# Optimization experiments

Hardware: AMD Instinct MI355X
Metric: run time of the kernel (lower is better)

Reference implementation:

```python
import jax, jax.numpy as jnp
import numpy as np


def _silu(x):
    return x * jax.nn.sigmoid(x)


def setup_inputs() -> dict:
    key = jax.random.key(0)
    ks = jax.random.split(key, 8)
    B, S, H, E, I, IS = 2, 1024, 2048, 64, 512, 1024
    s = 0.02  # weight init scale to keep activations in a sane range
    return {
        "hidden_states": jax.random.normal(ks[0], (B, S, H), jnp.float32),
        "gate_weight": jax.random.normal(ks[1], (E, H), jnp.float32) * s,   # router [E,H]
        "w_gate": jax.random.normal(ks[2], (E, H, I), jnp.float32) * s,
        "w_up": jax.random.normal(ks[3], (E, H, I), jnp.float32) * s,
        "w_down": jax.random.normal(ks[4], (E, I, H), jnp.float32) * s,
        "sw_gate": jax.random.normal(ks[5], (H, IS), jnp.float32) * s,
        "sw_up": jax.random.normal(ks[6], (H, IS), jnp.float32) * s,
        "sw_down": jax.random.normal(ks[7], (IS, H), jnp.float32) * s,
        "top_k": 6,
    }


def reference(hidden_states, gate_weight, w_gate, w_up, w_down,
              sw_gate, sw_up, sw_down, top_k):
    orig_shape = hidden_states.shape
    H = orig_shape[-1]
    x = hidden_states.reshape(-1, H)          # [T,H]
    T = x.shape[0]
    E = gate_weight.shape[0]

    # fp32 router (need_fp32_gate)
    logits = x.astype(jnp.float32) @ gate_weight.astype(jnp.float32).T   # [T,E]
    # sigmoid_routing_function: sigmoid -> normalize -> topk -> renormalize
    p = jax.nn.sigmoid(logits)
    p = p / jnp.sum(p, axis=-1, keepdims=True)
    topk_w, topk_idx = jax.lax.top_k(p, top_k)                           # [T,k]
    topk_w = topk_w / jnp.sum(topk_w, axis=-1, keepdims=True)            # renormalize

    # dense combine weights [T,E]: zero for unselected experts
    cw = jnp.zeros((T, E), x.dtype).at[jnp.arange(T)[:, None], topk_idx].set(
        topk_w.astype(x.dtype))

    # grouped SwiGLU expert FFN, combine weighted outputs; scan over experts
    # keeps peak memory at one [T,I] intermediate per step.
    def step(acc, ew):
        wg, wu, wd, c = ew                                               # c: [T]
        y = (_silu(x @ wg) * (x @ wu)) @ wd                              # [T,H]
        return acc + c[:, None] * y, None

    routed, _ = jax.lax.scan(step, jnp.zeros_like(x),
                             (w_gate, w_up, w_down, cw.T))

    # shared experts FFN over all tokens (returned separately, not reduced)
    shared_out = (_silu(x @ sw_gate) * (x @ sw_up)) @ sw_down            # [T,H]

    return shared_out, routed.reshape(orig_shape)
```

## Files before the change

### kernel.cpp

```cpp
#include <hip/hip_runtime.h>
#include <hip/hip_bf16.h>
#include <stdint.h>


#define H_DIM 2048
#define E_NUM 64
#define I_DIM 512
#define IS_DIM 1024
#define CAPR 288
#define TOPK_MAX 8
#define BK 64
#define LDP 68

typedef float f32x4 __attribute__((ext_vector_type(4)));
typedef __bf16 bf16x8 __attribute__((ext_vector_type(8)));

__device__ __forceinline__ uint16_t f2bf(float f) {
  union { float f; uint32_t u; } v;
  v.f = f;
  uint32_t r = (v.u + 0x7FFFu + ((v.u >> 16) & 1u)) >> 16;
  return (uint16_t)r;
}
__device__ __forceinline__ uint32_t pack2(float a, float b) {
  return (uint32_t)f2bf(a) | ((uint32_t)f2bf(b) << 16);
}
__device__ __forceinline__ float bf2f(uint16_t b) {
  union { uint32_t u; float f; } v;
  v.u = (uint32_t)b << 16;
  return v.f;
}

#define BAR()                                              \
  do {                                                     \
    asm volatile("s_waitcnt lgkmcnt(0)" ::: "memory");     \
    __builtin_amdgcn_s_barrier();                          \
    asm volatile("" ::: "memory");                         \
  } while (0)

__global__ __launch_bounds__(256) void router_kernel(
    const float* __restrict__ x, const float* __restrict__ gw,
    const int* __restrict__ topk_ptr, int* __restrict__ cnt,
    int* __restrict__ bucket, float* __restrict__ bw,
    uint16_t* __restrict__ xbK, const int T) {
  const int t = blockIdx.x;
  const int tid = threadIdx.x;
  __shared__ float xs[H_DIM];
  __shared__ float logits[E_NUM];
#pragma unroll
  for (int i = 0; i < 2; ++i) {
    int idx = tid + i * 256;
    *(float4*)(&xs[idx * 4]) = *(const float4*)(x + (size_t)t * H_DIM + idx * 4);
  }
  __syncthreads();
  {
    const float* p = &xs[tid * 8];
    uint4 o;
    o.x = pack2(p[0], p[1]);
    o.y = pack2(p[2], p[3]);
    o.z = pack2(p[4], p[5]);
    o.w = pack2(p[6], p[7]);
    *(uint4*)(xbK + (size_t)(tid >> 2) * T * 32 + (size_t)t * 32 +
              (tid & 3) * 8) = o;
  }
  const int lane = tid & 63, wid = tid >> 6;
  float xr[32];
#pragma unroll
  for (int it = 0; it < 32; ++it) xr[it] = xs[lane + 64 * it];
  for (int eo = 0; eo < 16; ++eo) {
    int e = wid + eo * 4;
    const float* g = gw + (size_t)e * H_DIM;
    float acc = 0.f;
#pragma unroll
    for (int it = 0; it < 32; ++it) acc += xr[it] * g[lane + 64 * it];
#pragma unroll
    for (int off = 32; off; off >>= 1) acc += __shfl_xor(acc, off);
    if (lane == 0) logits[e] = acc;
  }
  __syncthreads();
  if (wid == 0) {
    int k = topk_ptr[0];
    if (k > TOPK_MAX) k = TOPK_MAX;
    float v = 1.f / (1.f + expf(-logits[lane]));
    float s = 0.f, myw = 0.f;
    int mye = 0;
    for (int j = 0; j < k; ++j) {
      float m = v;
      int mi = lane;
#pragma unroll
      for (int off = 32; off; off >>= 1) {
        float ov = __shfl_xor(m, off);
        int oi = __shfl_xor(mi, off);
        if (ov > m || (ov == m && oi < mi)) { m = ov; mi = oi; }
      }
      if (lane == j) { myw = m; mye = mi; }
      if (lane == mi) v = -1e30f;
      s += m;
    }
    if (lane < k) {
      float w = myw / s;
      int pos = atomicAdd(&cnt[mye], 1);
      if (pos < CAPR) {
        bucket[mye * CAPR + pos] = t * 8 + lane;
        bw[mye * CAPR + pos] = w;
      }
    }
  }
}

__global__ __launch_bounds__(256) void gather_xe(
    const uint16_t* __restrict__ xbK, const int* __restrict__ cnt,
    const int* __restrict__ bucket, uint16_t* __restrict__ xe, const int T) {
  const int e = blockIdx.x;
  const int kgrp = blockIdx.y & 15, sgrp = blockIdx.y >> 4;
  const int tid = threadIdx.x;
  const int slot = sgrp * 64 + (tid & 63);
  const int kblk = kgrp * 4 + (tid >> 6);
  const int n_e = min(cnt[e], CAPR);
  if (slot >= n_e) return;
  const int t = bucket[e * CAPR + slot] >> 3;
  const uint4* src = (const uint4*)(xbK + (size_t)kblk * T * 32 + (size_t)t * 32);
  uint4* dst = (uint4*)(xe + (size_t)e * (64 * CAPR * 32) +
                        (size_t)kblk * (CAPR * 32) + (size_t)slot * 32);
#pragma unroll
  for (int j = 0; j < 4; ++j) dst[j] = src[j];
}

template <int BM, bool GATHER>
__global__ __launch_bounds__(256) void ffn_in(
    const uint16_t* __restrict__ A0, const float* __restrict__ Wg,
    const float* __restrict__ Wu, uint16_t* __restrict__ actO,
    const int* __restrict__ cnt, const int K, const int ldb, const int SLOTS) {
  constexpr int BN = 32;
  constexpr int MF = BM / 64;
  constexpr int NF = 2;

  int e = 0, nt, mt0, mtE, n_e;
  const float *Bg, *Bu;
  const uint16_t* AE;
  uint16_t* outE;
  if constexpr (GATHER) {
    e = blockIdx.x;
    nt = blockIdx.y;
    n_e = min(cnt[e], CAPR);
    mt0 = 0;
    mtE = (n_e + BM - 1) / BM;
    const size_t wo = (size_t)e * K * ldb;
    Bg = Wg + wo;
    Bu = Wu + wo;
    AE = A0 + (size_t)e * (64 * CAPR * 32);
    outE = actO + (size_t)e * ((I_DIM / 32) * CAPR * 32);
  } else {
    nt = blockIdx.x;
    mt0 = blockIdx.y;
    mtE = mt0 + 1;
    n_e = 1 << 30;
    Bg = Wg;
    Bu = Wu;
    AE = A0;
    outE = actO;
  }
  if (mt0 * BM >= n_e) return;

  __shared__ uint16_t Bgs[2][BN][LDP];
  __shared__ uint16_t Bus[2][BN][LDP];

  const int tid = threadIdx.x;
  const int cg4 = (tid & 7) * 4, kp = tid >> 3;
  const float* bgp = Bg + (size_t)(2 * kp) * ldb + nt * BN + cg4;
  const float* bup = Bu + (size_t)(2 * kp) * ldb + nt * BN + cg4;

  const int lane = tid & 63, wid = tid >> 6;
  const int fr = lane & 15, kg = lane >> 4;
  const int wrow = wid * (BM / 4);
  const size_t ldA = (size_t)SLOTS * 32;

  float4 g0, g1, u0, u1;
  const int NS = K / BK;

  for (int mt = mt0; mt < mtE; ++mt) {
    const uint16_t* ab[MF];
#pragma unroll
    for (int mf = 0; mf < MF; ++mf)
      ab[mf] = AE + (size_t)(mt * BM + wrow + mf * 16 + fr) * 32 + kg * 8;

    f32x4 accg[MF][NF] = {};
    f32x4 accu[MF][NF] = {};

    g0 = *(const float4*)bgp;
    g1 = *(const float4*)(bgp + ldb);
    u0 = *(const float4*)bup;
    u1 = *(const float4*)(bup + ldb);
    {
      const int k2 = 2 * kp;
      *(uint32_t*)(&Bgs[0][cg4 + 0][k2]) = pack2(g0.x, g1.x);
      *(uint32_t*)(&Bgs[0][cg4 + 1][k2]) = pack2(g0.y, g1.y);
      *(uint32_t*)(&Bgs[0][cg4 + 2][k2]) = pack2(g0.z, g1.z);
      *(uint32_t*)(&Bgs[0][cg4 + 3][k2]) = pack2(g0.w, g1.w);
      *(uint32_t*)(&Bus[0][cg4 + 0][k2]) = pack2(u0.x, u1.x);
      *(uint32_t*)(&Bus[0][cg4 + 1][k2]) = pack2(u0.y, u1.y);
      *(uint32_t*)(&Bus[0][cg4 + 2][k2]) = pack2(u0.z, u1.z);
      *(uint32_t*)(&Bus[0][cg4 + 3][k2]) = pack2(u0.w, u1.w);
    }
    if (NS > 1) {
      const float* g = bgp + (size_t)BK * ldb;
      g0 = *(const float4*)g;
      g1 = *(const float4*)(g + ldb);
      const float* u = bup + (size_t)BK * ldb;
      u0 = *(const float4*)u;
      u1 = *(const float4*)(u + ldb);
    }
    BAR();

    int b = 0;
    for (int s = 0; s < NS; ++s) {
      uint4 a[MF][2];
#pragma unroll
      for (int mf = 0; mf < MF; ++mf)
#pragma unroll
        for (int sl = 0; sl < 2; ++sl)
          a[mf][sl] = *(const uint4*)(ab[mf] + (size_t)(2 * s + sl) * ldA);
      if (s + 1 < NS) {
        const int k2 = 2 * kp;
        *(uint32_t*)(&Bgs[b ^ 1][cg4 + 0][k2]) = pack2(g0.x, g1.x);
        *(uint32_t*)(&Bgs[b ^ 1][cg4 + 1][k2]) = pack2(g0.y, g1.y);
        *(uint32_t*)(&Bgs[b ^ 1][cg4 + 2][k2]) = pack2(g0.z, g1.z);
        *(uint32_t*)(&Bgs[b ^ 1][cg4 + 3][k2]) = pack2(g0.w, g1.w);
        *(uint32_t*)(&Bus[b ^ 1][cg4 + 0][k2]) = pack2(u0.x, u1.x);
        *(uint32_t*)(&Bus[b ^ 1][cg4 + 1][k2]) = pack2(u0.y, u1.y);
        *(uint32_t*)(&Bus[b ^ 1][cg4 + 2][k2]) = pack2(u0.z, u1.z);
        *(uint32_t*)(&Bus[b ^ 1][cg4 + 3][k2]) = pack2(u0.w, u1.w);
      }
      if (s + 2 < NS) {
        const float* g = bgp + (size_t)((s + 2) * BK) * ldb;
        g0 = *(const float4*)g;
        g1 = *(const float4*)(g + ldb);
        const float* u = bup + (size_t)((s + 2) * BK) * ldb;
        u0 = *(const float4*)u;
        u1 = *(const float4*)(u + ldb);
      }
#pragma unroll
      for (int sl = 0; sl < 2; ++sl)
#pragma unroll
        for (int nf = 0; nf < NF; ++nf) {
          const bf16x8 bg = __builtin_bit_cast(
              bf16x8, *(const uint4*)(&Bgs[b][nf * 16 + fr][kg * 8 + sl * 32]));
          const bf16x8 bu = __builtin_bit_cast(
              bf16x8, *(const uint4*)(&Bus[b][nf * 16 + fr][kg * 8 + sl * 32]));
#pragma unroll
          for (int mf = 0; mf < MF; ++mf) {
            const bf16x8 af = __builtin_bit_cast(bf16x8, a[mf][sl]);
            accg[mf][nf] = __builtin_amdgcn_mfma_f32_16x16x32_bf16(
                af, bg, accg[mf][nf], 0, 0, 0);
            accu[mf][nf] = __builtin_amdgcn_mfma_f32_16x16x32_bf16(
                af, bu, accu[mf][nf], 0, 0, 0);
          }
        }
      BAR();
      b ^= 1;
    }

#pragma unroll
    for (int mf = 0; mf < MF; ++mf)
#pragma unroll
      for (int rr = 0; rr < 4; ++rr) {
        const int slot = mt * BM + wrow + mf * 16 + kg * 4 + rr;
        if (slot < n_e) {
          uint16_t* op = outE + (size_t)nt * ldA + (size_t)slot * 32 + fr;
#pragma unroll
          for (int nf = 0; nf < NF; ++nf) {
            const float g = accg[mf][nf][rr], u = accu[mf][nf][rr];
            op[nf * 16] = f2bf(g / (1.f + expf(-g)) * u);
          }
        }
      }
  }
}

template <int BM, bool GATHER>
__global__ __launch_bounds__(256) void ffn_down(
    const uint16_t* __restrict__ A0, const float* __restrict__ Wd,
    void* __restrict__ outp, const int* __restrict__ cnt,
    const int* __restrict__ bucket, const float* __restrict__ bw,
    const int K, const int SLOTS) {
  constexpr int BN = 64;
  constexpr int MF = BM / 64;
  constexpr int NF = 4;

  int e = 0, nt, mt0, mtE, n_e;
  const float* Bd;
  const uint16_t* AE;
  if constexpr (GATHER) {
    e = blockIdx.x;
    nt = blockIdx.y;
    n_e = min(cnt[e], CAPR);
    mt0 = 0;
    mtE = (n_e + BM - 1) / BM;
    AE = A0 + (size_t)e * ((I_DIM / 32) * CAPR * 32);
    Bd = Wd + (size_t)e * K * H_DIM;
  } else {
    nt = blockIdx.x;
    mt0 = blockIdx.y;
    mtE = mt0 + 1;
    n_e = 1 << 30;
    AE = A0;
    Bd = Wd;
  }
  if (mt0 * BM >= n_e) return;

  __shared__ uint16_t Bs[2][BN][LDP];

  const int tid = threadIdx.x;
  const int cg4 = (tid & 15) * 4, kp = tid >> 4;
  const float* bdp = Bd + (size_t)(2 * kp) * H_DIM + nt * BN + cg4;

  const int lane = tid & 63, wid = tid >> 6;
  const int fr = lane & 15, kg = lane >> 4;
  const int wrow = wid * (BM / 4);
  const size_t ldA = (size_t)SLOTS * 32;

  float4 d0[2], d1[2];
  const int NS = K / BK;

  for (int mt = mt0; mt < mtE; ++mt) {
    const uint16_t* ab[MF];
#pragma unroll
    for (int mf = 0; mf < MF; ++mf)
      ab[mf] = AE + (size_t)(mt * BM + wrow + mf * 16 + fr) * 32 + kg * 8;

    f32x4 acc[MF][NF] = {};

#pragma unroll
    for (int pp = 0; pp < 2; ++pp) {
      const float* d = bdp + (size_t)(2 * pp * 16) * H_DIM;
      d0[pp] = *(const float4*)d;
      d1[pp] = *(const float4*)(d + H_DIM);
    }
#pragma unroll
    for (int pp = 0; pp < 2; ++pp) {
      const int k2 = 2 * (kp + pp * 16);
      *(uint32_t*)(&Bs[0][cg4 + 0][k2]) = pack2(d0[pp].x, d1[pp].x);
      *(uint32_t*)(&Bs[0][cg4 + 1][k2]) = pack2(d0[pp].y, d1[pp].y);
      *(uint32_t*)(&Bs[0][cg4 + 2][k2]) = pack2(d0[pp].z, d1[pp].z);
      *(uint32_t*)(&Bs[0][cg4 + 3][k2]) = pack2(d0[pp].w, d1[pp].w);
    }
    if (NS > 1) {
#pragma unroll
      for (int pp = 0; pp < 2; ++pp) {
        const float* d = bdp + (size_t)(BK + 2 * pp * 16) * H_DIM;
        d0[pp] = *(const float4*)d;
        d1[pp] = *(const float4*)(d + H_DIM);
      }
    }
    BAR();

    int b = 0;
    for (int s = 0; s < NS; ++s) {
      uint4 a[MF][2];
#pragma unroll
      for (int mf = 0; mf < MF; ++mf)
#pragma unroll
        for (int sl = 0; sl < 2; ++sl)
          a[mf][sl] = *(const uint4*)(ab[mf] + (size_t)(2 * s + sl) * ldA);
      if (s + 1 < NS) {
#pragma unroll
        for (int pp = 0; pp < 2; ++pp) {
          const int k2 = 2 * (kp + pp * 16);
          *(uint32_t*)(&Bs[b ^ 1][cg4 + 0][k2]) = pack2(d0[pp].x, d1[pp].x);
          *(uint32_t*)(&Bs[b ^ 1][cg4 + 1][k2]) = pack2(d0[pp].y, d1[pp].y);
          *(uint32_t*)(&Bs[b ^ 1][cg4 + 2][k2]) = pack2(d0[pp].z, d1[pp].z);
          *(uint32_t*)(&Bs[b ^ 1][cg4 + 3][k2]) = pack2(d0[pp].w, d1[pp].w);
        }
      }
      if (s + 2 < NS) {
#pragma unroll
        for (int pp = 0; pp < 2; ++pp) {
          const float* d = bdp + (size_t)((s + 2) * BK + 2 * pp * 16) * H_DIM;
          d0[pp] = *(const float4*)d;
          d1[pp] = *(const float4*)(d + H_DIM);
        }
      }
#pragma unroll
      for (int sl = 0; sl < 2; ++sl)
#pragma unroll
        for (int nf = 0; nf < NF; ++nf) {
          const bf16x8 bf_ = __builtin_bit_cast(
              bf16x8, *(const uint4*)(&Bs[b][nf * 16 + fr][kg * 8 + sl * 32]));
#pragma unroll
          for (int mf = 0; mf < MF; ++mf) {
            const bf16x8 af = __builtin_bit_cast(bf16x8, a[mf][sl]);
            acc[mf][nf] = __builtin_amdgcn_mfma_f32_16x16x32_bf16(
                af, bf_, acc[mf][nf], 0, 0, 0);
          }
        }
      BAR();
      b ^= 1;
    }

    const int col0 = nt * BN + fr;
#pragma unroll
    for (int mf = 0; mf < MF; ++mf)
#pragma unroll
      for (int rr = 0; rr < 4; ++rr) {
        const int slot = mt * BM + wrow + mf * 16 + kg * 4 + rr;
        if constexpr (GATHER) {
          if (slot < n_e) {
            const int bv = bucket[e * CAPR + slot];
            const float w = bw[e * CAPR + slot];
            uint16_t* yb = (uint16_t*)outp + (size_t)bv * H_DIM + col0;
#pragma unroll
            for (int nf = 0; nf < NF; ++nf)
              yb[nf * 16] = f2bf(w * acc[mf][nf][rr]);
          }
        } else {
          float* op = (float*)outp + (size_t)slot * H_DIM + col0;
#pragma unroll
          for (int nf = 0; nf < NF; ++nf) op[nf * 16] = acc[mf][nf][rr];
        }
      }
  }
}

__global__ __launch_bounds__(256) void combine_kernel(
    const uint16_t* __restrict__ ybuf, const int* __restrict__ topk_ptr,
    float* __restrict__ routed) {
  const int t = blockIdx.x;
  const int tid = threadIdx.x;
  int k = topk_ptr[0];
  if (k > TOPK_MAX) k = TOPK_MAX;
  float acc[8] = {};
  const uint16_t* base = ybuf + (size_t)t * 8 * H_DIM + tid * 8;
  for (int j = 0; j < k; ++j) {
    uint4 v = *(const uint4*)(base + (size_t)j * H_DIM);
    const uint16_t* h = (const uint16_t*)&v;
#pragma unroll
    for (int i = 0; i < 8; ++i) acc[i] += bf2f(h[i]);
  }
  float* op = routed + (size_t)t * H_DIM + tid * 8;
  *(float4*)op = make_float4(acc[0], acc[1], acc[2], acc[3]);
  *(float4*)(op + 4) = make_float4(acc[4], acc[5], acc[6], acc[7]);
}

extern "C" void kernel_launch(void* const* d_in, const int* in_sizes, int n_in,
                              void* d_out, int out_size, void* d_ws, size_t ws_size,
                              hipStream_t stream) {
  const float* x = (const float*)d_in[0];
  const float* gw = (const float*)d_in[1];
  const float* w_gate = (const float*)d_in[2];
  const float* w_up = (const float*)d_in[3];
  const float* w_down = (const float*)d_in[4];
  const float* sw_gate = (const float*)d_in[5];
  const float* sw_up = (const float*)d_in[6];
  const float* sw_down = (const float*)d_in[7];
  const int* topk = (const int*)d_in[8];
  const int T = in_sizes[0] / H_DIM;

  float* shared_out = (float*)d_out;
  float* routed = shared_out + (size_t)T * H_DIM;

  char* ws = (char*)d_ws;
  size_t off = 0;
  auto take = [&](size_t b) {
    char* p = ws + off;
    off += (b + 255) & ~(size_t)255;
    return p;
  };
  uint16_t* xbK = (uint16_t*)take((size_t)T * H_DIM * 2);
  int* cnt = (int*)take(E_NUM * 4);
  int* bucket = (int*)take((size_t)E_NUM * CAPR * 4);
  float* bw = (float*)take((size_t)E_NUM * CAPR * 4);
  uint16_t* xe = (uint16_t*)take((size_t)E_NUM * 64 * CAPR * 32 * 2 + 65536);
  uint16_t* act = (uint16_t*)take((size_t)E_NUM * 16 * CAPR * 32 * 2 + 65536);
  uint16_t* s_act = (uint16_t*)take((size_t)(IS_DIM / 32) * T * 32 * 2);
  uint16_t* ybuf = (uint16_t*)take((size_t)T * 8 * H_DIM * 2);

  hipMemsetAsync(cnt, 0, E_NUM * 4, stream);

  router_kernel<<<T, 256, 0, stream>>>(x, gw, topk, cnt, bucket, bw, xbK, T);
  gather_xe<<<dim3(E_NUM, 16 * ((CAPR + 63) / 64)), 256, 0, stream>>>(
      xbK, cnt, bucket, xe, T);

  ffn_in<256, true><<<dim3(E_NUM, I_DIM / 32), 256, 0, stream>>>(
      xe, w_gate, w_up, act, cnt, H_DIM, I_DIM, CAPR);
  ffn_down<256, true><<<dim3(E_NUM, H_DIM / 64), 256, 0, stream>>>(
      act, w_down, (void*)ybuf, cnt, bucket, bw, I_DIM, CAPR);
  combine_kernel<<<T, 256, 0, stream>>>(ybuf, topk, routed);
  ffn_in<128, false><<<dim3(IS_DIM / 32, T / 128), 256, 0, stream>>>(
      xbK, sw_gate, sw_up, s_act, nullptr, H_DIM, IS_DIM, T);
  ffn_down<128, false><<<dim3(H_DIM / 64, T / 128), 256, 0, stream>>>(
      s_act, sw_down, (void*)shared_out, nullptr, nullptr, nullptr, IS_DIM, T);
}
```

Measured before the change: 440.5 us.

## Unroll GEMM k-loop by two with prefetched A registers and hardware bf16 pack

Both expert GEMM kernels (gate/up and down) now unroll the k-loop by two. They keep two register sets for the B tiles and two for the A fragments, so the A loads for the next step are issued before the barrier instead of at the top of each iteration. The software round-to-nearest bf16 conversion is replaced with the v_cvt_pk_bf16_f32 instruction. The aim is to hide global A-load latency behind the MFMAs and cut VALU work in the B packing. The cost is higher register pressure, which may lower occupancy. The loop assumes NS is even, or relies on guards when it is not.

```diff
diff --git a/kernel.cpp b/kernel.cpp
--- a/kernel.cpp
+++ b/kernel.cpp
@@ -23,6 +23,11 @@
 }
 __device__ __forceinline__ uint32_t pack2(float a, float b) {
   return (uint32_t)f2bf(a) | ((uint32_t)f2bf(b) << 16);
+}
+__device__ __forceinline__ uint32_t cvtpk(float a, float b) {
+  uint32_t r;
+  asm("v_cvt_pk_bf16_f32 %0, %1, %2" : "=v"(r) : "v"(a), "v"(b));
+  return r;
 }
 __device__ __forceinline__ float bf2f(uint16_t b) {
   union { uint32_t u; float f; } v;
@@ -174,89 +179,92 @@
   const int wrow = wid * (BM / 4);
   const size_t ldA = (size_t)SLOTS * 32;
 
-  float4 g0, g1, u0, u1;
+  struct BSet { float4 g0, g1, u0, u1; };
+  BSet bs0, bs1;
+  uint4 aA[MF][2], aB[MF][2];
+  const uint16_t* ab[MF];
+
+  auto issueB = [&](BSet& S, int kq) {
+    const float* g = bgp + (size_t)kq * ldb;
+    S.g0 = *(const float4*)g;
+    S.g1 = *(const float4*)(g + ldb);
+    const float* u = bup + (size_t)kq * ldb;
+    S.u0 = *(const float4*)u;
+    S.u1 = *(const float4*)(u + ldb);
+  };
+  auto packB = [&](int buf, const BSet& S) {
+    const int k2 = 2 * kp;
+    *(uint32_t*)(&Bgs[buf][cg4 + 0][k2]) = cvtpk(S.g0.x, S.g1.x);
+    *(uint32_t*)(&Bgs[buf][cg4 + 1][k2]) = cvtpk(S.g0.y, S.g1.y);
+    *(uint32_t*)(&Bgs[buf][cg4 + 2][k2]) = cvtpk(S.g0.z, S.g1.z);
+    *(uint32_t*)(&Bgs[buf][cg4 + 3][k2]) = cvtpk(S.g0.w, S.g1.w);
+    *(uint32_t*)(&Bus[buf][cg4 + 0][k2]) = cvtpk(S.u0.x, S.u1.x);
+    *(uint32_t*)(&Bus[buf][cg4 + 1][k2]) = cvtpk(S.u0.y, S.u1.y);
+    *(uint32_t*)(&Bus[buf][cg4 + 2][k2]) = cvtpk(S.u0.z, S.u1.z);
+    *(uint32_t*)(&Bus[buf][cg4 + 3][k2]) = cvtpk(S.u0.w, S.u1.w);
+  };
+  auto issueA = [&](uint4 (&A)[MF][2], int s) {
+#pragma unroll
+    for (int mf = 0; mf < MF; ++mf)
+#pragma unroll
+      for (int sl = 0; sl < 2; ++sl)
+        A[mf][sl] = *(const uint4*)(ab[mf] + (size_t)(2 * s + sl) * ldA);
+  };
+
+  f32x4 accg[MF][NF];
+  f32x4 accu[MF][NF];
+
+  auto mfmaStep = [&](int buf, uint4 (&A)[MF][2]) {
+#pragma unroll
+    for (int sl = 0; sl < 2; ++sl)
+#pragma unroll
+      for (int nf = 0; nf < NF; ++nf) {
+        const bf16x8 bg = __builtin_bit_cast(
+            bf16x8, *(const uint4*)(&Bgs[buf][nf * 16 + fr][kg * 8 + sl * 32]));
+        const bf16x8 bu = __builtin_bit_cast(
+            bf16x8, *(const uint4*)(&Bus[buf][nf * 16 + fr][kg * 8 + sl * 32]));
+#pragma unroll
+        for (int mf = 0; mf < MF; ++mf) {
+          const bf16x8 af = __builtin_bit_cast(bf16x8, A[mf][sl]);
+          accg[mf][nf] = __builtin_amdgcn_mfma_f32_16x16x32_bf16(
+              af, bg, accg[mf][nf], 0, 0, 0);
+          accu[mf][nf] = __builtin_amdgcn_mfma_f32_16x16x32_bf16(
+              af, bu, accu[mf][nf], 0, 0, 0);
+        }
+      }
+  };
+
   const int NS = K / BK;
-
   for (int mt = mt0; mt < mtE; ++mt) {
-    const uint16_t* ab[MF];
 #pragma unroll
     for (int mf = 0; mf < MF; ++mf)
       ab[mf] = AE + (size_t)(mt * BM + wrow + mf * 16 + fr) * 32 + kg * 8;
-
-    f32x4 accg[MF][NF] = {};
-    f32x4 accu[MF][NF] = {};
-
-    g0 = *(const float4*)bgp;
-    g1 = *(const float4*)(bgp + ldb);
-    u0 = *(const float4*)bup;
-    u1 = *(const float4*)(bup + ldb);
-    {
-      const int k2 = 2 * kp;
-      *(uint32_t*)(&Bgs[0][cg4 + 0][k2]) = pack2(g0.x, g1.x);
-      *(uint32_t*)(&Bgs[0][cg4 + 1][k2]) = pack2(g0.y, g1.y);
-      *(uint32_t*)(&Bgs[0][cg4 + 2][k2]) = pack2(g0.z, g1.z);
-      *(uint32_t*)(&Bgs[0][cg4 + 3][k2]) = pack2(g0.w, g1.w);
-      *(uint32_t*)(&Bus[0][cg4 + 0][k2]) = pack2(u0.x, u1.x);
-      *(uint32_t*)(&Bus[0][cg4 + 1][k2]) = pack2(u0.y, u1.y);
-      *(uint32_t*)(&Bus[0][cg4 + 2][k2]) = pack2(u0.z, u1.z);
-      *(uint32_t*)(&Bus[0][cg4 + 3][k2]) = pack2(u0.w, u1.w);
-    }
-    if (NS > 1) {
-      const float* g = bgp + (size_t)BK * ldb;
-      g0 = *(const float4*)g;
-      g1 = *(const float4*)(g + ldb);
-      const float* u = bup + (size_t)BK * ldb;
-      u0 = *(const float4*)u;
-      u1 = *(const float4*)(u + ldb);
-    }
+#pragma unroll
+    for (int mf = 0; mf < MF; ++mf)
+#pragma unroll
+      for (int nf = 0; nf < NF; ++nf) {
+        accg[mf][nf] = (f32x4){0.f, 0.f, 0.f, 0.f};
+        accu[mf][nf] = (f32x4){0.f, 0.f, 0.f, 0.f};
+      }
+
+    issueB(bs0, 0);
+    issueA(aA, 0);
+    packB(0, bs0);
+    issueB(bs1, BK);
+    issueA(aB, 1);
     BAR();
 
-    int b = 0;
-    for (int s = 0; s < NS; ++s) {
-      uint4 a[MF][2];
-#pragma unroll
-      for (int mf = 0; mf < MF; ++mf)
-#pragma unroll
-        for (int sl = 0; sl < 2; ++sl)
-          a[mf][sl] = *(const uint4*)(ab[mf] + (size_t)(2 * s + sl) * ldA);
-      if (s + 1 < NS) {
-        const int k2 = 2 * kp;
-        *(uint32_t*)(&Bgs[b ^ 1][cg4 + 0][k2]) = pack2(g0.x, g1.x);
-        *(uint32_t*)(&Bgs[b ^ 1][cg4 + 1][k2]) = pack2(g0.y, g1.y);
-        *(uint32_t*)(&Bgs[b ^ 1][cg4 + 2][k2]) = pack2(g0.z, g1.z);
-        *(uint32_t*)(&Bgs[b ^ 1][cg4 + 3][k2]) = pack2(g0.w, g1.w);
-        *(uint32_t*)(&Bus[b ^ 1][cg4 + 0][k2]) = pack2(u0.x, u1.x);
-        *(uint32_t*)(&Bus[b ^ 1][cg4 + 1][k2]) = pack2(u0.y, u1.y);
-        *(uint32_t*)(&Bus[b ^ 1][cg4 + 2][k2]) = pack2(u0.z, u1.z);
-        *(uint32_t*)(&Bus[b ^ 1][cg4 + 3][k2]) = pack2(u0.w, u1.w);
-      }
-      if (s + 2 < NS) {
-        const float* g = bgp + (size_t)((s + 2) * BK) * ldb;
-        g0 = *(const float4*)g;
-        g1 = *(const float4*)(g + ldb);
-        const float* u = bup + (size_t)((s + 2) * BK) * ldb;
-        u0 = *(const float4*)u;
-        u1 = *(const float4*)(u + ldb);
-      }
-#pragma unroll
-      for (int sl = 0; sl < 2; ++sl)
-#pragma unroll
-        for (int nf = 0; nf < NF; ++nf) {
-          const bf16x8 bg = __builtin_bit_cast(
-              bf16x8, *(const uint4*)(&Bgs[b][nf * 16 + fr][kg * 8 + sl * 32]));
-          const bf16x8 bu = __builtin_bit_cast(
-              bf16x8, *(const uint4*)(&Bus[b][nf * 16 + fr][kg * 8 + sl * 32]));
-#pragma unroll
-          for (int mf = 0; mf < MF; ++mf) {
-            const bf16x8 af = __builtin_bit_cast(bf16x8, a[mf][sl]);
-            accg[mf][nf] = __builtin_amdgcn_mfma_f32_16x16x32_bf16(
-                af, bg, accg[mf][nf], 0, 0, 0);
-            accu[mf][nf] = __builtin_amdgcn_mfma_f32_16x16x32_bf16(
-                af, bu, accu[mf][nf], 0, 0, 0);
-          }
-        }
+    for (int s = 0; s < NS; s += 2) {
+      if (s + 1 < NS) packB(1, bs1);
+      if (s + 2 < NS) issueB(bs0, (s + 2) * BK);
+      mfmaStep(0, aA);
+      if (s + 2 < NS) issueA(aA, s + 2);
       BAR();
-      b ^= 1;
+      if (s + 2 < NS) packB(0, bs0);
+      if (s + 3 < NS) issueB(bs1, (s + 3) * BK);
+      mfmaStep(1, aB);
+      if (s + 3 < NS) issueA(aB, s + 3);
+      BAR();
     }
 
 #pragma unroll
@@ -318,82 +326,83 @@
   const int wrow = wid * (BM / 4);
   const size_t ldA = (size_t)SLOTS * 32;
 
-  float4 d0[2], d1[2];
-  const int NS = K / BK;
-
-  for (int mt = mt0; mt < mtE; ++mt) {
-    const uint16_t* ab[MF];
-#pragma unroll
-    for (int mf = 0; mf < MF; ++mf)
-      ab[mf] = AE + (size_t)(mt * BM + wrow + mf * 16 + fr) * 32 + kg * 8;
-
-    f32x4 acc[MF][NF] = {};
-
+  struct DSet { float4 d0[2], d1[2]; };
+  DSet bs0, bs1;
+  uint4 aA[MF][2], aB[MF][2];
+  const uint16_t* ab[MF];
+
+  auto issueB = [&](DSet& S, int kq) {
 #pragma unroll
     for (int pp = 0; pp < 2; ++pp) {
-      const float* d = bdp + (size_t)(2 * pp * 16) * H_DIM;
-      d0[pp] = *(const float4*)d;
-      d1[pp] = *(const float4*)(d + H_DIM);
+      const float* d = bdp + (size_t)(kq + 2 * pp * 16) * H_DIM;
+      S.d0[pp] = *(const float4*)d;
+      S.d1[pp] = *(const float4*)(d + H_DIM);
     }
+  };
+  auto packB = [&](int buf, const DSet& S) {
 #pragma unroll
     for (int pp = 0; pp < 2; ++pp) {
       const int k2 = 2 * (kp + pp * 16);
-      *(uint32_t*)(&Bs[0][cg4 + 0][k2]) = pack2(d0[pp].x, d1[pp].x);
-      *(uint32_t*)(&Bs[0][cg4 + 1][k2]) = pack2(d0[pp].y, d1[pp].y);
-      *(uint32_t*)(&Bs[0][cg4 + 2][k2]) = pack2(d0[pp].z, d1[pp].z);
-      *(uint32_t*)(&Bs[0][cg4 + 3][k2]) = pack2(d0[pp].w, d1[pp].w);
+      *(uint32_t*)(&Bs[buf][cg4 + 0][k2]) = cvtpk(S.d0[pp].x, S.d1[pp].x);
+      *(uint32_t*)(&Bs[buf][cg4 + 1][k2]) = cvtpk(S.d0[pp].y, S.d1[pp].y);
+      *(uint32_t*)(&Bs[buf][cg4 + 2][k2]) = cvtpk(S.d0[pp].z, S.d1[pp].z);
+      *(uint32_t*)(&Bs[buf][cg4 + 3][k2]) = cvtpk(S.d0[pp].w, S.d1[pp].w);
     }
-    if (NS > 1) {
-#pragma unroll
-      for (int pp = 0; pp < 2; ++pp) {
-        const float* d = bdp + (size_t)(BK + 2 * pp * 16) * H_DIM;
-        d0[pp] = *(const float4*)d;
-        d1[pp] = *(const float4*)(d + H_DIM);
-      }
-    }
+  };
+  auto issueA = [&](uint4 (&A)[MF][2], int s) {
+#pragma unroll
+    for (int mf = 0; mf < MF; ++mf)
+#pragma unroll
+      for (int sl = 0; sl < 2; ++sl)
+        A[mf][sl] = *(const uint4*)(ab[mf] + (size_t)(2 * s + sl) * ldA);
+  };
+
+  f32x4 acc[MF][NF];
+
+  auto mfmaStep = [&](int buf, uint4 (&A)[MF][2]) {
+#pragma unroll
+    for (int sl = 0; sl < 2; ++sl)
+#pragma unroll
+      for (int nf = 0; nf < NF; ++nf) {
+        const bf16x8 bf_ = __builtin_bit_cast(
+            bf16x8, *(const uint4*)(&Bs[buf][nf * 16 + fr][kg * 8 + sl * 32]));
+#pragma unroll
+        for (int mf = 0; mf < MF; ++mf) {
+          const bf16x8 af = __builtin_bit_cast(bf16x8, A[mf][sl]);
+          acc[mf][nf] = __builtin_amdgcn_mfma_f32_16x16x32_bf16(
+              af, bf_, acc[mf][nf], 0, 0, 0);
+        }
+      }
+  };
+
+  const int NS = K / BK;
+  for (int mt = mt0; mt < mtE; ++mt) {
+#pragma unroll
+    for (int mf = 0; mf < MF; ++mf)
+      ab[mf] = AE + (size_t)(mt * BM + wrow + mf * 16 + fr) * 32 + kg * 8;
+#pragma unroll
+    for (int mf = 0; mf < MF; ++mf)
+#pragma unroll
+      for (int nf = 0; nf < NF; ++nf) acc[mf][nf] = (f32x4){0.f, 0.f, 0.f, 0.f};
+
+    issueB(bs0, 0);
+    issueA(aA, 0);
+    packB(0, bs0);
+    issueB(bs1, BK);
+    issueA(aB, 1);
     BAR();
 
-    int b = 0;
-    for (int s = 0; s < NS; ++s) {
-      uint4 a[MF][2];
-#pragma unroll
-      for (int mf = 0; mf < MF; ++mf)
-#pragma unroll
-        for (int sl = 0; sl < 2; ++sl)
-          a[mf][sl] = *(const uint4*)(ab[mf] + (size_t)(2 * s + sl) * ldA);
-      if (s + 1 < NS) {
-#pragma unroll
-        for (int pp = 0; pp < 2; ++pp) {
-          const int k2 = 2 * (kp + pp * 16);
-          *(uint32_t*)(&Bs[b ^ 1][cg4 + 0][k2]) = pack2(d0[pp].x, d1[pp].x);
-          *(uint32_t*)(&Bs[b ^ 1][cg4 + 1][k2]) = pack2(d0[pp].y, d1[pp].y);
-          *(uint32_t*)(&Bs[b ^ 1][cg4 + 2][k2]) = pack2(d0[pp].z, d1[pp].z);
-          *(uint32_t*)(&Bs[b ^ 1][cg4 + 3][k2]) = pack2(d0[pp].w, d1[pp].w);
-        }
-      }
-      if (s + 2 < NS) {
-#pragma unroll
-        for (int pp = 0; pp < 2; ++pp) {
-          const float* d = bdp + (size_t)((s + 2) * BK + 2 * pp * 16) * H_DIM;
-          d0[pp] = *(const float4*)d;
-          d1[pp] = *(const float4*)(d + H_DIM);
-        }
-      }
-#pragma unroll
-      for (int sl = 0; sl < 2; ++sl)
-#pragma unroll
-        for (int nf = 0; nf < NF; ++nf) {
-          const bf16x8 bf_ = __builtin_bit_cast(
-              bf16x8, *(const uint4*)(&Bs[b][nf * 16 + fr][kg * 8 + sl * 32]));
-#pragma unroll
-          for (int mf = 0; mf < MF; ++mf) {
-            const bf16x8 af = __builtin_bit_cast(bf16x8, a[mf][sl]);
-            acc[mf][nf] = __builtin_amdgcn_mfma_f32_16x16x32_bf16(
-                af, bf_, acc[mf][nf], 0, 0, 0);
-          }
-        }
+    for (int s = 0; s < NS; s += 2) {
+      if (s + 1 < NS) packB(1, bs1);
+      if (s + 2 < NS) issueB(bs0, (s + 2) * BK);
+      mfmaStep(0, aA);
+      if (s + 2 < NS) issueA(aA, s + 2);
       BAR();
-      b ^= 1;
+      if (s + 2 < NS) packB(0, bs0);
+      if (s + 3 < NS) issueB(bs1, (s + 3) * BK);
+      mfmaStep(1, aB);
+      if (s + 3 < NS) issueA(aB, s + 3);
+      BAR();
     }
 
     const int col0 = nt * BN + fr;
```

After: 474.5 us. 1.08x slower.

## Pre-convert shared weights to bf16 K-blocked layout and use LDS-free dense GEMMs

Applied to the files above, without the earlier changes.

Adds a conversion kernel that transposes the shared-expert fp32 weights into bf16 in a K-blocked layout each call. New dense_in/dense_down kernels then load A and B fragments straight from global memory into registers with two-stage prefetch, dropping LDS staging and barriers. The routed-expert kernels are de-templated and their bf16 packing moves to the hardware v_cvt_pk_bf16_f32 instruction. This trades an extra pass over the shared weights and more workspace for simpler, barrier-free shared GEMMs. Register-only B loads may reuse data less and put more pressure on L2.

```diff
diff --git a/kernel.cpp b/kernel.cpp
--- a/kernel.cpp
+++ b/kernel.cpp
@@ -23,6 +23,11 @@
 }
 __device__ __forceinline__ uint32_t pack2(float a, float b) {
   return (uint32_t)f2bf(a) | ((uint32_t)f2bf(b) << 16);
+}
+__device__ __forceinline__ uint32_t cvtpk(float a, float b) {
+  uint32_t r;
+  asm("v_cvt_pk_bf16_f32 %0, %1, %2" : "=v"(r) : "v"(a), "v"(b));
+  return r;
 }
 __device__ __forceinline__ float bf2f(uint16_t b) {
   union { uint32_t u; float f; } v;
@@ -125,59 +130,215 @@
   for (int j = 0; j < 4; ++j) dst[j] = src[j];
 }
 
-template <int BM, bool GATHER>
-__global__ __launch_bounds__(256) void ffn_in(
-    const uint16_t* __restrict__ A0, const float* __restrict__ Wg,
-    const float* __restrict__ Wu, uint16_t* __restrict__ actO,
-    const int* __restrict__ cnt, const int K, const int ldb, const int SLOTS) {
-  constexpr int BN = 32;
-  constexpr int MF = BM / 64;
-  constexpr int NF = 2;
-
-  int e = 0, nt, mt0, mtE, n_e;
-  const float *Bg, *Bu;
-  const uint16_t* AE;
-  uint16_t* outE;
-  if constexpr (GATHER) {
-    e = blockIdx.x;
-    nt = blockIdx.y;
-    n_e = min(cnt[e], CAPR);
-    mt0 = 0;
-    mtE = (n_e + BM - 1) / BM;
-    const size_t wo = (size_t)e * K * ldb;
-    Bg = Wg + wo;
-    Bu = Wu + wo;
-    AE = A0 + (size_t)e * (64 * CAPR * 32);
-    outE = actO + (size_t)e * ((I_DIM / 32) * CAPR * 32);
-  } else {
-    nt = blockIdx.x;
-    mt0 = blockIdx.y;
-    mtE = mt0 + 1;
-    n_e = 1 << 30;
-    Bg = Wg;
-    Bu = Wu;
-    AE = A0;
-    outE = actO;
-  }
-  if (mt0 * BM >= n_e) return;
+__global__ __launch_bounds__(256) void cvt_wT(const float* __restrict__ src,
+                                              uint16_t* __restrict__ dst,
+                                              const int N) {
+  const int n0 = blockIdx.x * 64, kb = blockIdx.y;
+  __shared__ uint16_t ts[32][72];
+  const int tid = threadIdx.x;
+  const int r = tid >> 3, c8 = (tid & 7) * 8;
+  const float* s = src + (size_t)(kb * 32 + r) * N + n0 + c8;
+  float4 v0 = *(const float4*)s, v1 = *(const float4*)(s + 4);
+  *(uint32_t*)&ts[r][c8 + 0] = cvtpk(v0.x, v0.y);
+  *(uint32_t*)&ts[r][c8 + 2] = cvtpk(v0.z, v0.w);
+  *(uint32_t*)&ts[r][c8 + 4] = cvtpk(v1.x, v1.y);
+  *(uint32_t*)&ts[r][c8 + 6] = cvtpk(v1.z, v1.w);
+  __syncthreads();
+  const int n = tid >> 2, kq = (tid & 3) * 8;
+  uint16_t o[8];
+#pragma unroll
+  for (int j = 0; j < 8; ++j) o[j] = ts[kq + j][n];
+  *(uint4*)(dst + ((size_t)kb * N + n0 + n) * 32 + kq) = *(uint4*)o;
+}
+
+__global__ __launch_bounds__(256) void dense_in(
+    const uint16_t* __restrict__ xbK, const uint16_t* __restrict__ BgT,
+    const uint16_t* __restrict__ BuT, uint16_t* __restrict__ s_actK,
+    const int T) {
+  const int nt = blockIdx.x, mt = blockIdx.y;
+  const int tid = threadIdx.x, lane = tid & 63, wid = tid >> 6;
+  const int fr = lane & 15, kg = lane >> 4;
+  const int m0 = mt * 128 + wid * 32, n0 = nt * 32;
+  const size_t sA = (size_t)T * 32, sB = (size_t)IS_DIM * 32;
+
+  const uint16_t *pa[2], *pg[2], *pu[2];
+#pragma unroll
+  for (int i = 0; i < 2; ++i) {
+    pa[i] = xbK + (size_t)(m0 + i * 16 + fr) * 32 + kg * 8;
+    pg[i] = BgT + (size_t)(n0 + i * 16 + fr) * 32 + kg * 8;
+    pu[i] = BuT + (size_t)(n0 + i * 16 + fr) * 32 + kg * 8;
+  }
+
+  f32x4 accg[2][2] = {};
+  f32x4 accu[2][2] = {};
+  uint4 a0[2], g0[2], u0[2], a1[2], g1[2], u1[2];
+
+#pragma unroll
+  for (int i = 0; i < 2; ++i) {
+    a0[i] = *(const uint4*)pa[i];
+    g0[i] = *(const uint4*)pg[i];
+    u0[i] = *(const uint4*)pu[i];
+  }
+
+  const int NS = H_DIM / 32;
+  for (int s = 0; s < NS; s += 2) {
+#pragma unroll
+    for (int i = 0; i < 2; ++i) {
+      a1[i] = *(const uint4*)(pa[i] + sA);
+      g1[i] = *(const uint4*)(pg[i] + sB);
+      u1[i] = *(const uint4*)(pu[i] + sB);
+    }
+#pragma unroll
+    for (int nf = 0; nf < 2; ++nf)
+#pragma unroll
+      for (int mf = 0; mf < 2; ++mf) {
+        const bf16x8 af = __builtin_bit_cast(bf16x8, a0[mf]);
+        accg[mf][nf] = __builtin_amdgcn_mfma_f32_16x16x32_bf16(
+            af, __builtin_bit_cast(bf16x8, g0[nf]), accg[mf][nf], 0, 0, 0);
+        accu[mf][nf] = __builtin_amdgcn_mfma_f32_16x16x32_bf16(
+            af, __builtin_bit_cast(bf16x8, u0[nf]), accu[mf][nf], 0, 0, 0);
+      }
+#pragma unroll
+    for (int i = 0; i < 2; ++i) {
+      pa[i] += 2 * sA;
+      pg[i] += 2 * sB;
+      pu[i] += 2 * sB;
+    }
+    if (s + 2 < NS) {
+#pragma unroll
+      for (int i = 0; i < 2; ++i) {
+        a0[i] = *(const uint4*)pa[i];
+        g0[i] = *(const uint4*)pg[i];
+        u0[i] = *(const uint4*)pu[i];
+      }
+    }
+#pragma unroll
+    for (int nf = 0; nf < 2; ++nf)
+#pragma unroll
+      for (int mf = 0; mf < 2; ++mf) {
+        const bf16x8 af = __builtin_bit_cast(bf16x8, a1[mf]);
+        accg[mf][nf] = __builtin_amdgcn_mfma_f32_16x16x32_bf16(
+            af, __builtin_bit_cast(bf16x8, g1[nf]), accg[mf][nf], 0, 0, 0);
+        accu[mf][nf] = __builtin_amdgcn_mfma_f32_16x16x32_bf16(
+            af, __builtin_bit_cast(bf16x8, u1[nf]), accu[mf][nf], 0, 0, 0);
+      }
+  }
+
+#pragma unroll
+  for (int mf = 0; mf < 2; ++mf)
+#pragma unroll
+    for (int rr = 0; rr < 4; ++rr) {
+      const int t = m0 + mf * 16 + kg * 4 + rr;
+      uint16_t* op = s_actK + ((size_t)nt * T + t) * 32 + fr;
+#pragma unroll
+      for (int nf = 0; nf < 2; ++nf) {
+        const float g = accg[mf][nf][rr], u = accu[mf][nf][rr];
+        op[nf * 16] = f2bf(g / (1.f + expf(-g)) * u);
+      }
+    }
+}
+
+__global__ __launch_bounds__(256) void dense_down(
+    const uint16_t* __restrict__ s_actK, const uint16_t* __restrict__ BdT,
+    float* __restrict__ outp, const int T) {
+  const int nt = blockIdx.x, mt = blockIdx.y;
+  const int tid = threadIdx.x, lane = tid & 63, wid = tid >> 6;
+  const int fr = lane & 15, kg = lane >> 4;
+  const int m0 = mt * 128 + wid * 32, n0 = nt * 32;
+  const size_t sA = (size_t)T * 32, sB = (size_t)H_DIM * 32;
+
+  const uint16_t *pa[2], *pd[2];
+#pragma unroll
+  for (int i = 0; i < 2; ++i) {
+    pa[i] = s_actK + (size_t)(m0 + i * 16 + fr) * 32 + kg * 8;
+    pd[i] = BdT + (size_t)(n0 + i * 16 + fr) * 32 + kg * 8;
+  }
+
+  f32x4 acc[2][2] = {};
+  uint4 a0[2], d0[2], a1[2], d1[2];
+#pragma unroll
+  for (int i = 0; i < 2; ++i) {
+    a0[i] = *(const uint4*)pa[i];
+    d0[i] = *(const uint4*)pd[i];
+  }
+
+  const int NS = IS_DIM / 32;
+  for (int s = 0; s < NS; s += 2) {
+#pragma unroll
+    for (int i = 0; i < 2; ++i) {
+      a1[i] = *(const uint4*)(pa[i] + sA);
+      d1[i] = *(const uint4*)(pd[i] + sB);
+    }
+#pragma unroll
+    for (int nf = 0; nf < 2; ++nf)
+#pragma unroll
+      for (int mf = 0; mf < 2; ++mf)
+        acc[mf][nf] = __builtin_amdgcn_mfma_f32_16x16x32_bf16(
+            __builtin_bit_cast(bf16x8, a0[mf]),
+            __builtin_bit_cast(bf16x8, d0[nf]), acc[mf][nf], 0, 0, 0);
+#pragma unroll
+    for (int i = 0; i < 2; ++i) {
+      pa[i] += 2 * sA;
+      pd[i] += 2 * sB;
+    }
+    if (s + 2 < NS) {
+#pragma unroll
+      for (int i = 0; i < 2; ++i) {
+        a0[i] = *(const uint4*)pa[i];
+        d0[i] = *(const uint4*)pd[i];
+      }
+    }
+#pragma unroll
+    for (int nf = 0; nf < 2; ++nf)
+#pragma unroll
+      for (int mf = 0; mf < 2; ++mf)
+        acc[mf][nf] = __builtin_amdgcn_mfma_f32_16x16x32_bf16(
+            __builtin_bit_cast(bf16x8, a1[mf]),
+            __builtin_bit_cast(bf16x8, d1[nf]), acc[mf][nf], 0, 0, 0);
+  }
+
+#pragma unroll
+  for (int mf = 0; mf < 2; ++mf)
+#pragma unroll
+    for (int rr = 0; rr < 4; ++rr) {
+      const int t = m0 + mf * 16 + kg * 4 + rr;
+      float* op = outp + (size_t)t * H_DIM + n0 + fr;
+#pragma unroll
+      for (int nf = 0; nf < 2; ++nf) op[nf * 16] = acc[mf][nf][rr];
+    }
+}
+
+__global__ __launch_bounds__(256) void moe_in(
+    const uint16_t* __restrict__ xe, const float* __restrict__ Wg,
+    const float* __restrict__ Wu, uint16_t* __restrict__ act,
+    const int* __restrict__ cnt) {
+  constexpr int BM = 256, MF = 4, NF = 2, BN = 32;
+  const int e = blockIdx.x, nt = blockIdx.y;
+  const int n_e = min(cnt[e], CAPR);
+  const int mtE = (n_e + BM - 1) / BM;
+  const size_t wo = (size_t)e * H_DIM * I_DIM;
+  const float* Bg = Wg + wo;
+  const float* Bu = Wu + wo;
+  const uint16_t* AE = xe + (size_t)e * (64 * CAPR * 32);
+  uint16_t* outE = act + (size_t)e * ((I_DIM / 32) * CAPR * 32);
 
   __shared__ uint16_t Bgs[2][BN][LDP];
   __shared__ uint16_t Bus[2][BN][LDP];
 
   const int tid = threadIdx.x;
   const int cg4 = (tid & 7) * 4, kp = tid >> 3;
-  const float* bgp = Bg + (size_t)(2 * kp) * ldb + nt * BN + cg4;
-  const float* bup = Bu + (size_t)(2 * kp) * ldb + nt * BN + cg4;
+  const float* bgp = Bg + (size_t)(2 * kp) * I_DIM + nt * BN + cg4;
+  const float* bup = Bu + (size_t)(2 * kp) * I_DIM + nt * BN + cg4;
 
   const int lane = tid & 63, wid = tid >> 6;
   const int fr = lane & 15, kg = lane >> 4;
   const int wrow = wid * (BM / 4);
-  const size_t ldA = (size_t)SLOTS * 32;
+  const size_t ldA = (size_t)CAPR * 32;
 
   float4 g0, g1, u0, u1;
-  const int NS = K / BK;
-
-  for (int mt = mt0; mt < mtE; ++mt) {
+  const int NS = H_DIM / BK;
+
+  for (int mt = 0; mt < mtE; ++mt) {
     const uint16_t* ab[MF];
 #pragma unroll
     for (int mf = 0; mf < MF; ++mf)
@@ -187,27 +348,27 @@
     f32x4 accu[MF][NF] = {};
 
     g0 = *(const float4*)bgp;
-    g1 = *(const float4*)(bgp + ldb);
+    g1 = *(const float4*)(bgp + I_DIM);
     u0 = *(const float4*)bup;
-    u1 = *(const float4*)(bup + ldb);
+    u1 = *(const float4*)(bup + I_DIM);
     {
       const int k2 = 2 * kp;
-      *(uint32_t*)(&Bgs[0][cg4 + 0][k2]) = pack2(g0.x, g1.x);
-      *(uint32_t*)(&Bgs[0][cg4 + 1][k2]) = pack2(g0.y, g1.y);
-      *(uint32_t*)(&Bgs[0][cg4 + 2][k2]) = pack2(g0.z, g1.z);
-      *(uint32_t*)(&Bgs[0][cg4 + 3][k2]) = pack2(g0.w, g1.w);
-      *(uint32_t*)(&Bus[0][cg4 + 0][k2]) = pack2(u0.x, u1.x);
-      *(uint32_t*)(&Bus[0][cg4 + 1][k2]) = pack2(u0.y, u1.y);
-      *(uint32_t*)(&Bus[0][cg4 + 2][k2]) = pack2(u0.z, u1.z);
-      *(uint32_t*)(&Bus[0][cg4 + 3][k2]) = pack2(u0.w, u1.w);
-    }
-    if (NS > 1) {
-      const float* g = bgp + (size_t)BK * ldb;
+      *(uint32_t*)(&Bgs[0][cg4 + 0][k2]) = cvtpk(g0.x, g1.x);
+      *(uint32_t*)(&Bgs[0][cg4 + 1][k2]) = cvtpk(g0.y, g1.y);
+      *(uint32_t*)(&Bgs[0][cg4 + 2][k2]) = cvtpk(g0.z, g1.z);
+      *(uint32_t*)(&Bgs[0][cg4 + 3][k2]) = cvtpk(g0.w, g1.w);
+      *(uint32_t*)(&Bus[0][cg4 + 0][k2]) = cvtpk(u0.x, u1.x);
+      *(uint32_t*)(&Bus[0][cg4 + 1][k2]) = cvtpk(u0.y, u1.y);
+      *(uint32_t*)(&Bus[0][cg4 + 2][k2]) = cvtpk(u0.z, u1.z);
+      *(uint32_t*)(&Bus[0][cg4 + 3][k2]) = cvtpk(u0.w, u1.w);
+    }
+    {
+      const float* g = bgp + (size_t)BK * I_DIM;
       g0 = *(const float4*)g;
-      g1 = *(const float4*)(g + ldb);
-      const float* u = bup + (size_t)BK * ldb;
+      g1 = *(const float4*)(g + I_DIM);
+      const float* u = bup + (size_t)BK * I_DIM;
       u0 = *(const float4*)u;
-      u1 = *(const float4*)(u + ldb);
+      u1 = *(const float4*)(u + I_DIM);
     }
     BAR();
 
@@ -221,22 +382,22 @@
           a[mf][sl] = *(const uint4*)(ab[mf] + (size_t)(2 * s + sl) * ldA);
       if (s + 1 < NS) {
         const int k2 = 2 * kp;
-        *(uint32_t*)(&Bgs[b ^ 1][cg4 + 0][k2]) = pack2(g0.x, g1.x);
-        *(uint32_t*)(&Bgs[b ^ 1][cg4 + 1][k2]) = pack2(g0.y, g1.y);
-        *(uint32_t*)(&Bgs[b ^ 1][cg4 + 2][k2]) = pack2(g0.z, g1.z);
-        *(uint32_t*)(&Bgs[b ^ 1][cg4 + 3][k2]) = pack2(g0.w, g1.w);
-        *(uint32_t*)(&Bus[b ^ 1][cg4 + 0][k2]) = pack2(u0.x, u1.x);
-        *(uint32_t*)(&Bus[b ^ 1][cg4 + 1][k2]) = pack2(u0.y, u1.y);
-        *(uint32_t*)(&Bus[b ^ 1][cg4 + 2][k2]) = pack2(u0.z, u1.z);
-        *(uint32_t*)(&Bus[b ^ 1][cg4 + 3][k2]) = pack2(u0.w, u1.w);
+        *(uint32_t*)(&Bgs[b ^ 1][cg4 + 0][k2]) = cvtpk(g0.x, g1.x);
+        *(uint32_t*)(&Bgs[b ^ 1][cg4 + 1][k2]) = cvtpk(g0.y, g1.y);
+        *(uint32_t*)(&Bgs[b ^ 1][cg4 + 2][k2]) = cvtpk(g0.z, g1.z);
+        *(uint32_t*)(&Bgs[b ^ 1][cg4 + 3][k2]) = cvtpk(g0.w, g1.w);
+        *(uint32_t*)(&Bus[b ^ 1][cg4 + 0][k2]) = cvtpk(u0.x, u1.x);
+        *(uint32_t*)(&Bus[b ^ 1][cg4 + 1][k2]) = cvtpk(u0.y, u1.y);
+        *(uint32_t*)(&Bus[b ^ 1][cg4 + 2][k2]) = cvtpk(u0.z, u1.z);
+        *(uint32_t*)(&Bus[b ^ 1][cg4 + 3][k2]) = cvtpk(u0.w, u1.w);
       }
       if (s + 2 < NS) {
-        const float* g = bgp + (size_t)((s + 2) * BK) * ldb;
+        const float* g = bgp + (size_t)((s + 2) * BK) * I_DIM;
         g0 = *(const float4*)g;
-        g1 = *(const float4*)(g + ldb);
-        const float* u = bup + (size_t)((s + 2) * BK) * ldb;
+        g1 = *(const float4*)(g + I_DIM);
+        const float* u = bup + (size_t)((s + 2) * BK) * I_DIM;
         u0 = *(const float4*)u;
-        u1 = *(const float4*)(u + ldb);
+        u1 = *(const float4*)(u + I_DIM);
       }
 #pragma unroll
       for (int sl = 0; sl < 2; ++sl)
@@ -276,36 +437,16 @@
   }
 }
 
-template <int BM, bool GATHER>
-__global__ __launch_bounds__(256) void ffn_down(
-    const uint16_t* __restrict__ A0, const float* __restrict__ Wd,
-    void* __restrict__ outp, const int* __restrict__ cnt,
-    const int* __restrict__ bucket, const float* __restrict__ bw,
-    const int K, const int SLOTS) {
-  constexpr int BN = 64;
-  constexpr int MF = BM / 64;
-  constexpr int NF = 4;
-
-  int e = 0, nt, mt0, mtE, n_e;
-  const float* Bd;
-  const uint16_t* AE;
-  if constexpr (GATHER) {
-    e = blockIdx.x;
-    nt = blockIdx.y;
-    n_e = min(cnt[e], CAPR);
-    mt0 = 0;
-    mtE = (n_e + BM - 1) / BM;
-    AE = A0 + (size_t)e * ((I_DIM / 32) * CAPR * 32);
-    Bd = Wd + (size_t)e * K * H_DIM;
-  } else {
-    nt = blockIdx.x;
-    mt0 = blockIdx.y;
-    mtE = mt0 + 1;
-    n_e = 1 << 30;
-    AE = A0;
-    Bd = Wd;
-  }
-  if (mt0 * BM >= n_e) return;
+__global__ __launch_bounds__(256) void moe_down(
+    const uint16_t* __restrict__ act, const float* __restrict__ Wd,
+    uint16_t* __restrict__ ybuf, const int* __restrict__ cnt,
+    const int* __restrict__ bucket, const float* __restrict__ bw) {
+  constexpr int BM = 256, MF = 4, NF = 4, BN = 64;
+  const int e = blockIdx.x, nt = blockIdx.y;
+  const int n_e = min(cnt[e], CAPR);
+  const int mtE = (n_e + BM - 1) / BM;
+  const uint16_t* AE = act + (size_t)e * ((I_DIM / 32) * CAPR * 32);
+  const float* Bd = Wd + (size_t)e * I_DIM * H_DIM;
 
   __shared__ uint16_t Bs[2][BN][LDP];
 
@@ -316,12 +457,12 @@
   const int lane = tid & 63, wid = tid >> 6;
   const int fr = lane & 15, kg = lane >> 4;
   const int wrow = wid * (BM / 4);
-  const size_t ldA = (size_t)SLOTS * 32;
+  const size_t ldA = (size_t)CAPR * 32;
 
   float4 d0[2], d1[2];
-  const int NS = K / BK;
-
-  for (int mt = mt0; mt < mtE; ++mt) {
+  const int NS = I_DIM / BK;
+
+  for (int mt = 0; mt < mtE; ++mt) {
     const uint16_t* ab[MF];
 #pragma unroll
     for (int mf = 0; mf < MF; ++mf)
@@ -338,18 +479,16 @@
 #pragma unroll
     for (int pp = 0; pp < 2; ++pp) {
       const int k2 = 2 * (kp + pp * 16);
-      *(uint32_t*)(&Bs[0][cg4 + 0][k2]) = pack2(d0[pp].x, d1[pp].x);
-      *(uint32_t*)(&Bs[0][cg4 + 1][k2]) = pack2(d0[pp].y, d1[pp].y);
-      *(uint32_t*)(&Bs[0][cg4 + 2][k2]) = pack2(d0[pp].z, d1[pp].z);
-      *(uint32_t*)(&Bs[0][cg4 + 3][k2]) = pack2(d0[pp].w, d1[pp].w);
-    }
-    if (NS > 1) {
-#pragma unroll
-      for (int pp = 0; pp < 2; ++pp) {
-        const float* d = bdp + (size_t)(BK + 2 * pp * 16) * H_DIM;
-        d0[pp] = *(const float4*)d;
-        d1[pp] = *(const float4*)(d + H_DIM);
-      }
+      *(uint32_t*)(&Bs[0][cg4 + 0][k2]) = cvtpk(d0[pp].x, d1[pp].x);
+      *(uint32_t*)(&Bs[0][cg4 + 1][k2]) = cvtpk(d0[pp].y, d1[pp].y);
+      *(uint32_t*)(&Bs[0][cg4 + 2][k2]) = cvtpk(d0[pp].z, d1[pp].z);
+      *(uint32_t*)(&Bs[0][cg4 + 3][k2]) = cvtpk(d0[pp].w, d1[pp].w);
+    }
+#pragma unroll
+    for (int pp = 0; pp < 2; ++pp) {
+      const float* d = bdp + (size_t)(BK + 2 * pp * 16) * H_DIM;
+      d0[pp] = *(const float4*)d;
+      d1[pp] = *(const float4*)(d + H_DIM);
     }
     BAR();
 
@@ -365,10 +504,10 @@
 #pragma unroll
         for (int pp = 0; pp < 2; ++pp) {
           const int k2 = 2 * (kp + pp * 16);
-          *(uint32_t*)(&Bs[b ^ 1][cg4 + 0][k2]) = pack2(d0[pp].x, d1[pp].x);
-          *(uint32_t*)(&Bs[b ^ 1][cg4 + 1][k2]) = pack2(d0[pp].y, d1[pp].y);
-          *(uint32_t*)(&Bs[b ^ 1][cg4 + 2][k2]) = pack2(d0[pp].z, d1[pp].z);
-          *(uint32_t*)(&Bs[b ^ 1][cg4 + 3][k2]) = pack2(d0[pp].w, d1[pp].w);
+          *(uint32_t*)(&Bs[b ^ 1][cg4 + 0][k2]) = cvtpk(d0[pp].x, d1[pp].x);
+          *(uint32_t*)(&Bs[b ^ 1][cg4 + 1][k2]) = cvtpk(d0[pp].y, d1[pp].y);
+          *(uint32_t*)(&Bs[b ^ 1][cg4 + 2][k2]) = cvtpk(d0[pp].z, d1[pp].z);
+          *(uint32_t*)(&Bs[b ^ 1][cg4 + 3][k2]) = cvtpk(d0[pp].w, d1[pp].w);
         }
       }
       if (s + 2 < NS) {
@@ -402,19 +541,12 @@
 #pragma unroll
       for (int rr = 0; rr < 4; ++rr) {
         const int slot = mt * BM + wrow + mf * 16 + kg * 4 + rr;
-        if constexpr (GATHER) {
-          if (slot < n_e) {
-            const int bv = bucket[e * CAPR + slot];
-            const float w = bw[e * CAPR + slot];
-            uint16_t* yb = (uint16_t*)outp + (size_t)bv * H_DIM + col0;
-#pragma unroll
-            for (int nf = 0; nf < NF; ++nf)
-              yb[nf * 16] = f2bf(w * acc[mf][nf][rr]);
-          }
-        } else {
-          float* op = (float*)outp + (size_t)slot * H_DIM + col0;
-#pragma unroll
-          for (int nf = 0; nf < NF; ++nf) op[nf * 16] = acc[mf][nf][rr];
+        if (slot < n_e) {
+          const int bv = bucket[e * CAPR + slot];
+          const float w = bw[e * CAPR + slot];
+          uint16_t* yb = ybuf + (size_t)bv * H_DIM + col0;
+#pragma unroll
+          for (int nf = 0; nf < NF; ++nf) yb[nf * 16] = f2bf(w * acc[mf][nf][rr]);
         }
       }
   }
@@ -470,8 +602,11 @@
   float* bw = (float*)take((size_t)E_NUM * CAPR * 4);
   uint16_t* xe = (uint16_t*)take((size_t)E_NUM * 64 * CAPR * 32 * 2 + 65536);
   uint16_t* act = (uint16_t*)take((size_t)E_NUM * 16 * CAPR * 32 * 2 + 65536);
-  uint16_t* s_act = (uint16_t*)take((size_t)(IS_DIM / 32) * T * 32 * 2);
+  uint16_t* s_actK = (uint16_t*)take((size_t)(IS_DIM / 32) * T * 32 * 2);
   uint16_t* ybuf = (uint16_t*)take((size_t)T * 8 * H_DIM * 2);
+  uint16_t* sgT = (uint16_t*)take((size_t)H_DIM * IS_DIM * 2);
+  uint16_t* suT = (uint16_t*)take((size_t)H_DIM * IS_DIM * 2);
+  uint16_t* sdT = (uint16_t*)take((size_t)IS_DIM * H_DIM * 2);
 
   hipMemsetAsync(cnt, 0, E_NUM * 4, stream);
 
@@ -479,13 +614,17 @@
   gather_xe<<<dim3(E_NUM, 16 * ((CAPR + 63) / 64)), 256, 0, stream>>>(
       xbK, cnt, bucket, xe, T);
 
-  ffn_in<256, true><<<dim3(E_NUM, I_DIM / 32), 256, 0, stream>>>(
-      xe, w_gate, w_up, act, cnt, H_DIM, I_DIM, CAPR);
-  ffn_down<256, true><<<dim3(E_NUM, H_DIM / 64), 256, 0, stream>>>(
-      act, w_down, (void*)ybuf, cnt, bucket, bw, I_DIM, CAPR);
+  cvt_wT<<<dim3(IS_DIM / 64, H_DIM / 32), 256, 0, stream>>>(sw_gate, sgT, IS_DIM);
+  cvt_wT<<<dim3(IS_DIM / 64, H_DIM / 32), 256, 0, stream>>>(sw_up, suT, IS_DIM);
+  cvt_wT<<<dim3(H_DIM / 64, IS_DIM / 32), 256, 0, stream>>>(sw_down, sdT, H_DIM);
+
+  moe_in<<<dim3(E_NUM, I_DIM / 32), 256, 0, stream>>>(xe, w_gate, w_up, act, cnt);
+  moe_down<<<dim3(E_NUM, H_DIM / 64), 256, 0, stream>>>(act, w_down, ybuf, cnt,
+                                                        bucket, bw);
   combine_kernel<<<T, 256, 0, stream>>>(ybuf, topk, routed);
-  ffn_in<128, false><<<dim3(IS_DIM / 32, T / 128), 256, 0, stream>>>(
-      xbK, sw_gate, sw_up, s_act, nullptr, H_DIM, IS_DIM, T);
-  ffn_down<128, false><<<dim3(H_DIM / 64, T / 128), 256, 0, stream>>>(
-      s_act, sw_down, (void*)shared_out, nullptr, nullptr, nullptr, IS_DIM, T);
-}
+
+  dense_in<<<dim3(IS_DIM / 32, T / 128), 256, 0, stream>>>(xbK, sgT, suT,
+                                                           s_actK, T);
+  dense_down<<<dim3(H_DIM / 32, T / 128), 256, 0, stream>>>(s_actK, sdT,
+                                                            shared_out, T);
+}
```

Result: slower. 550.3 us (+24.9%).
